# Kernel optimization log

Hardware: AMD Instinct MI355X
Metric: run time of the kernel (lower is better)

Reference implementation:

```python
import jax, jax.numpy as jnp
import numpy as np

DIM, HEADS, HEAD_DIM = 1024, 16, 64
B, S = 2, 1024
LAMBDA = 4.0
EPS = 1e-6


def setup_inputs() -> dict:
    key = jax.random.key(0)
    ks = jax.random.split(key, 7)
    sc = 1.0 / np.sqrt(DIM)
    return {
        "x": jax.random.normal(ks[0], (B, S, DIM), jnp.float32),
        "qkv_w": jax.random.normal(ks[1], (3 * DIM, DIM), jnp.float32) * sc,
        "qkv_b": jax.random.normal(ks[2], (3 * DIM,), jnp.float32) * 0.01,
        "proj_w": jax.random.normal(ks[3], (DIM, DIM), jnp.float32) * sc,
        "proj_b": jax.random.normal(ks[4], (DIM,), jnp.float32) * 0.01,
        "dwc_w": jax.random.normal(ks[5], (DIM, 1, 3), jnp.float32) * 0.3,
        "dwc_b": jax.random.normal(ks[6], (DIM,), jnp.float32) * 0.01,
    }


def _l1_dist(q, k):
    # q,k: [B,H,S,Dh] -> pairwise L1 distance [B,H,S,S].
    # Accumulate over head_dim with a (rematerialized) scan so we never
    # materialize the [B,H,S,S,Dh] broadcast tensor.
    qT = jnp.moveaxis(q, -1, 0)  # [Dh,B,H,S]
    kT = jnp.moveaxis(k, -1, 0)

    def step(acc, qk):
        qd, kd = qk  # [B,H,S]
        return acc + jnp.abs(qd[..., :, None] - kd[..., None, :]), None

    init = jnp.zeros(q.shape[:-1] + (k.shape[-2],), q.dtype)
    dist, _ = jax.lax.scan(jax.checkpoint(step), init, (qT, kT))
    return dist


def reference(x, qkv_w, qkv_b, proj_w, proj_b, dwc_w, dwc_b):
    Bq, Sq, C = x.shape
    # qkv projection -> q,k,v each [B,H,S,Dh]
    qkv = (x @ qkv_w.T + qkv_b).reshape(Bq, Sq, 3, HEADS, HEAD_DIM)
    qkv = jnp.transpose(qkv, (2, 0, 3, 1, 4))
    q, k, v = qkv[0], qkv[1], qkv[2]

    # exact Laplacian (L1-distance) kernel attention, row-normalized
    dist = _l1_dist(q, k)                       # [B,H,S,S]
    kern = jnp.exp(-LAMBDA * dist / HEAD_DIM)   # mean-L1 scaling
    attn = kern / (jnp.sum(kern, axis=-1, keepdims=True) + EPS)
    global_attn = jnp.einsum("bhij,bhjd->bhid", attn, v)

    # depthwise conv1d local branch on v (channel order = head-major)
    v1d = jnp.transpose(v, (0, 1, 3, 2)).reshape(Bq, C, Sq)  # [B,C,S]
    local = jax.lax.conv_general_dilated(
        v1d, dwc_w, window_strides=(1,), padding=((1, 1),),
        feature_group_count=C, dimension_numbers=("NCH", "OIH", "NCH"))
    local = local + dwc_b[None, :, None]
    local = jnp.transpose(local.reshape(Bq, HEADS, HEAD_DIM, Sq), (0, 1, 3, 2))

    y = global_attn + local                      # [B,H,S,Dh]
    y = jnp.transpose(y, (0, 2, 1, 3)).reshape(Bq, Sq, C)
    return y @ proj_w.T + proj_b
```

## Files before the change

kernel.cpp:

```cpp
#include <hip/hip_runtime.h>

#define DIMC 1024
#define HEADS 16
#define HD 64
#define BATCH 2
#define SEQ 1024
#define NQKV 3072

typedef _Float16 f16;
typedef _Float16 half8 __attribute__((ext_vector_type(8)));
typedef _Float16 half4v __attribute__((ext_vector_type(4)));
typedef float floatx4 __attribute__((ext_vector_type(4)));

__device__ __forceinline__ void gld16(const void* g, void* l) {
  __builtin_amdgcn_global_load_lds((const __attribute__((address_space(1))) void*)g,
                                   (__attribute__((address_space(3))) void*)l, 16, 0, 0);
}

__device__ __forceinline__ unsigned sadU8(unsigned a, unsigned b, unsigned c) {
#if __has_builtin(__builtin_amdgcn_sad_u8)
  return __builtin_amdgcn_sad_u8(a, b, c);
#else
  unsigned d;
  asm("v_sad_u8 %0, %1, %2, %3" : "=v"(d) : "v"(a), "v"(b), "v"(c));
  return d;
#endif
}

__global__ __launch_bounds__(256) void cvt_kernel(
    const float* __restrict__ x, const float* __restrict__ wq, const float* __restrict__ wp,
    f16* __restrict__ x16, f16* __restrict__ wq16, f16* __restrict__ wp16)
{
  int bid = blockIdx.x;
  const float* src; f16* dst; int base;
  if (bid < 512)        { src = x;  dst = x16;  base = bid; }
  else if (bid < 1280)  { src = wq; dst = wq16; base = bid - 512; }
  else                  { src = wp; dst = wp16; base = bid - 1280; }
  long long i0 = (long long)base*1024 + threadIdx.x;
#pragma unroll
  for (int k2 = 0; k2 < 4; ++k2) {
    long long i = i0 + k2*256;
    float4 v = ((const float4*)src)[i];
    half4v h; h[0]=(f16)v.x; h[1]=(f16)v.y; h[2]=(f16)v.z; h[3]=(f16)v.w;
    *(half4v*)(dst + i*4) = h;
  }
}

template<int TM, int TN, int BK, int MW, int MODE>
__global__ __launch_bounds__(256, MW) void gemm_kernel(
    const f16* __restrict__ A, const f16* __restrict__ Bw, const float* __restrict__ bias,
    unsigned char* __restrict__ q8, unsigned char* __restrict__ k8, f16* __restrict__ vT,
    float* __restrict__ outp, int K)
{
  constexpr int MT = TM / 32;
  constexpr int NT = TN / 32;
  constexpr int G  = BK / 8;
  __shared__ f16 As[TM*BK];
  __shared__ f16 Bs[TN*BK];
  const int tid = threadIdx.x;
  const int wave = tid >> 6, lane = tid & 63;
  const int lq = lane >> 4, li = lane & 15;
  const int m0 = blockIdx.y * TM, n0 = blockIdx.x * TN;
  const int wm = (wave & 1) * (TM/2), wn = (wave >> 1) * (TN/2);
  floatx4 acc[MT][NT] = {};

  const int kIters = K / BK;
  for (int kt = 0; kt < kIters; ++kt) {
    __syncthreads();
#pragma unroll
    for (int r = 0; r < TM*BK/2048; ++r) {
      int slot = r*256 + tid;
      int row = slot / G, c = slot % G, g = c ^ (row & (G-1));
      gld16(A + (size_t)(m0+row)*K + kt*BK + g*8, As + slot*8);
    }
#pragma unroll
    for (int r = 0; r < TN*BK/2048; ++r) {
      int slot = r*256 + tid;
      int row = slot / G, c = slot % G, g = c ^ (row & (G-1));
      gld16(Bw + (size_t)(n0+row)*K + kt*BK + g*8, Bs + slot*8);
    }
    __syncthreads();
#pragma unroll
    for (int ks = 0; ks < BK/32; ++ks) {
      half8 af[MT], bf[NT];
      int kc = ks*4 + lq;
#pragma unroll
      for (int t = 0; t < MT; ++t) {
        int am = wm + t*16 + li;
        af[t] = *(const half8*)&As[am*BK + (kc ^ (am & (G-1)))*8];
      }
#pragma unroll
      for (int t = 0; t < NT; ++t) {
        int bn = wn + t*16 + li;
        bf[t] = *(const half8*)&Bs[bn*BK + (kc ^ (bn & (G-1)))*8];
      }
#pragma unroll
      for (int mt = 0; mt < MT; ++mt)
#pragma unroll
        for (int nt = 0; nt < NT; ++nt)
          acc[mt][nt] = __builtin_amdgcn_mfma_f32_16x16x32_f16(af[mt], bf[nt], acc[mt][nt], 0, 0, 0);
    }
  }

#pragma unroll
  for (int mt = 0; mt < MT; ++mt) {
#pragma unroll
    for (int nt = 0; nt < NT; ++nt) {
      int f = n0 + wn + nt*16 + li;
      float bb = bias[f];
      if (MODE == 0) {
        int which = f >> 10, cc = f & 1023, h = cc >> 6, d = cc & 63;
        int t0 = m0 + wm + mt*16 + lq*4;
        int b = t0 >> 10, s0 = t0 & 1023;
        if (which == 2) {
          half4v hv;
#pragma unroll
          for (int r = 0; r < 4; ++r) hv[r] = (f16)(acc[mt][nt][r] + bb);
          *(half4v*)&vT[((size_t)((b*HEADS + h)*HD + d))*SEQ + s0] = hv;
        } else {
          unsigned char* dst = (which == 0) ? q8 : k8;
#pragma unroll
          for (int r = 0; r < 4; ++r) {
            float v = acc[mt][nt][r] + bb;
            int u = (int)floorf(v * 16.0f + 128.5f);
            u = u < 0 ? 0 : (u > 255 ? 255 : u);
            dst[((size_t)((b*HEADS + h)*SEQ + s0 + r))*HD + d] = (unsigned char)u;
          }
        }
      } else {
#pragma unroll
        for (int r = 0; r < 4; ++r) {
          int t = m0 + wm + mt*16 + lq*4 + r;
          outp[(size_t)t*DIMC + f] = acc[mt][nt][r] + bb;
        }
      }
    }
  }
}

__global__ __launch_bounds__(256, 4) void attn_kernel(
    const unsigned char* __restrict__ q8g, const unsigned char* __restrict__ k8g,
    const f16* __restrict__ vTg, const float* __restrict__ dwcw, const float* __restrict__ dwcb,
    f16* __restrict__ y16)
{
  __shared__ unsigned char q8s[32*64];
  __shared__ unsigned char k8s[128*64];
  __shared__ f16 vTs[64*128];
  __shared__ f16 sfrag[8*64*8];
  __shared__ float rspart[32*16];
  __shared__ float rowsum[32];

  const int tid = threadIdx.x;
  const int lin = blockIdx.x + 16 * blockIdx.y;
  const int bh = (lin & 7) * 4 + ((lin >> 3) & 3);
  const int i0 = (lin >> 5) * 32;
  const int lane = tid & 63, wave = tid >> 6;
  const int lq = lane >> 4, li = lane & 15;
  const int iL = tid & 15, jt = tid >> 4;
  const int ksj = jt >> 2, qj = jt & 3;

  {
    if (tid < 128)
      gld16(q8g + ((size_t)(bh*SEQ) + i0)*HD + tid*16, q8s + tid*16);
  }
  __syncthreads();

  unsigned qr[2][16];
#pragma unroll
  for (int n = 0; n < 2; ++n)
#pragma unroll
    for (int c4 = 0; c4 < 4; ++c4) {
      uint4 t = *(const uint4*)&q8s[(iL + n*16)*64 + c4*16];
      qr[n][c4*4+0] = t.x; qr[n][c4*4+1] = t.y; qr[n][c4*4+2] = t.z; qr[n][c4*4+3] = t.w;
    }

  float rs[2] = {0.f, 0.f};
  floatx4 pacc[2] = {};

  for (int jb = 0; jb < 8; ++jb) {
    const int j0 = jb * 128;
    __syncthreads();
#pragma unroll
    for (int r = 0; r < 2; ++r) {
      int slot = r*256 + tid;
      gld16(k8g + ((size_t)(bh*SEQ) + j0)*HD + slot*16, k8s + slot*16);
    }
#pragma unroll
    for (int r = 0; r < 4; ++r) {
      int slot = r*256 + tid;
      int d = slot >> 4, c = slot & 15, sc = c ^ (d & 7);
      gld16(vTg + ((size_t)(bh*HD) + d)*SEQ + j0 + sc*8, vTs + slot*8);
    }
    __syncthreads();

    unsigned sacc[2][8] = {};
#pragma unroll
    for (int c4 = 0; c4 < 4; ++c4) {
      uint4 kk[8];
#pragma unroll
      for (int jj = 0; jj < 8; ++jj)
        kk[jj] = *(const uint4*)&k8s[(jt*8 + jj)*64 + c4*16];
#pragma unroll
      for (int n = 0; n < 2; ++n)
#pragma unroll
        for (int jj = 0; jj < 8; ++jj) {
          sacc[n][jj] = sadU8(qr[n][c4*4+0], kk[jj].x, sacc[n][jj]);
          sacc[n][jj] = sadU8(qr[n][c4*4+1], kk[jj].y, sacc[n][jj]);
          sacc[n][jj] = sadU8(qr[n][c4*4+2], kk[jj].z, sacc[n][jj]);
          sacc[n][jj] = sadU8(qr[n][c4*4+3], kk[jj].w, sacc[n][jj]);
        }
    }
#pragma unroll
    for (int n = 0; n < 2; ++n) {
      half8 sv;
#pragma unroll
      for (int jj = 0; jj < 8; ++jj) {
        float sf = exp2f(-0.0056355275f * (float)sacc[n][jj]);
        rs[n] += sf;
        sv[jj] = (f16)sf;
      }
      *(half8*)&sfrag[((n*4 + ksj)*64 + qj*16 + iL)*8] = sv;
    }
    __syncthreads();

#pragma unroll
    for (int ks = 0; ks < 4; ++ks) {
      half8 a0 = *(const half8*)&sfrag[((0*4 + ks)*64 + lane)*8];
      half8 a1 = *(const half8*)&sfrag[((1*4 + ks)*64 + lane)*8];
      int d = wave*16 + li;
      int kc = ks*4 + lq;
      half8 bfr = *(const half8*)&vTs[d*128 + (kc ^ (d & 7))*8];
      pacc[0] = __builtin_amdgcn_mfma_f32_16x16x32_f16(a0, bfr, pacc[0], 0, 0, 0);
      pacc[1] = __builtin_amdgcn_mfma_f32_16x16x32_f16(a1, bfr, pacc[1], 0, 0, 0);
    }
  }

#pragma unroll
  for (int n = 0; n < 2; ++n) rspart[(iL + n*16)*16 + jt] = rs[n];
  __syncthreads();
  if (tid < 32) {
    float s = 0.f;
#pragma unroll
    for (int t = 0; t < 16; ++t) s += rspart[tid*16 + t];
    rowsum[tid] = s + 1e-6f;
  }
  __syncthreads();

  const int b = bh >> 4, h = bh & 15;
  {
    int d = wave*16 + li;
    int c = h*64 + d;
    float w0 = dwcw[c*3+0], w1 = dwcw[c*3+1], w2 = dwcw[c*3+2], cb = dwcb[c];
    const f16* vrow = vTg + ((size_t)(bh*HD) + d)*SEQ;
#pragma unroll
    for (int mt = 0; mt < 2; ++mt) {
      int s0 = i0 + mt*16 + lq*4;
      float vv[6];
#pragma unroll
      for (int e = 0; e < 6; ++e) {
        int s = s0 - 1 + e;
        vv[e] = (s >= 0 && s < SEQ) ? (float)vrow[s] : 0.f;
      }
#pragma unroll
      for (int r = 0; r < 4; ++r) {
        int ii = mt*16 + lq*4 + r;
        float val = pacc[mt][r] / rowsum[ii];
        val += w0*vv[r] + w1*vv[r+1] + w2*vv[r+2] + cb;
        int s = i0 + ii;
        y16[((size_t)(b*SEQ + s))*DIMC + c] = (f16)val;
      }
    }
  }
}

extern "C" void kernel_launch(void* const* d_in, const int* in_sizes, int n_in,
                              void* d_out, int out_size, void* d_ws, size_t ws_size,
                              hipStream_t stream) {
  const float* x      = (const float*)d_in[0];
  const float* qkv_w  = (const float*)d_in[1];
  const float* qkv_b  = (const float*)d_in[2];
  const float* proj_w = (const float*)d_in[3];
  const float* proj_b = (const float*)d_in[4];
  const float* dwc_w  = (const float*)d_in[5];
  const float* dwc_b  = (const float*)d_in[6];
  float* out = (float*)d_out;

  char* ws = (char*)d_ws;
  f16* x16  = (f16*)(ws);
  f16* wq16 = (f16*)(ws + (4ll<<20));
  f16* wp16 = (f16*)(ws + (10ll<<20));
  unsigned char* q8 = (unsigned char*)(ws + (12ll<<20));
  unsigned char* k8 = (unsigned char*)(ws + (14ll<<20));
  f16* vT   = (f16*)(ws + (16ll<<20));
  f16* y16  = (f16*)(ws + (20ll<<20));

  cvt_kernel<<<1536, 256, 0, stream>>>(x, qkv_w, proj_w, x16, wq16, wp16);
  gemm_kernel<128,128,128,2,0><<<dim3(24, 16), 256, 0, stream>>>(x16, wq16, qkv_b, q8, k8, vT, nullptr, DIMC);
  attn_kernel<<<dim3(16, 64), 256, 0, stream>>>(q8, k8, vT, dwc_w, dwc_b, y16);
  gemm_kernel<64,64,128,4,1><<<dim3(16, 32), 256, 0, stream>>>(y16, wp16, proj_b, nullptr, nullptr, nullptr, out, DIMC);
}
```

Baseline: 150.1 us.

## Double-buffer K tiles, load V fragments directly to registers, swizzle K LDS

The attention kernel now double-buffers the K tile in LDS, prefetching the next block while the current one is processed. This drops one of the two barriers per iteration. V is no longer staged through LDS: each lane loads its MFMA B-fragment straight from global memory into registers, and the sfrag buffer is double-buffered so the single remaining barrier is enough. K rows are XOR-swizzled across 16-byte chunks to reduce LDS bank conflicts. The risks are global-load latency on V sitting directly in front of the MFMAs, and the correctness of a single barrier per iteration with async LDS loads.

```diff
diff --git a/kernel.cpp b/kernel.cpp
--- a/kernel.cpp
+++ b/kernel.cpp
@@ -144,9 +144,8 @@
     f16* __restrict__ y16)
 {
   __shared__ unsigned char q8s[32*64];
-  __shared__ unsigned char k8s[128*64];
-  __shared__ f16 vTs[64*128];
-  __shared__ f16 sfrag[8*64*8];
+  __shared__ unsigned char k8s[2][128*64];
+  __shared__ f16 sfrag[2][8*64*8];
   __shared__ float rspart[32*16];
   __shared__ float rowsum[32];
 
@@ -158,10 +157,17 @@
   const int lq = lane >> 4, li = lane & 15;
   const int iL = tid & 15, jt = tid >> 4;
   const int ksj = jt >> 2, qj = jt & 3;
+  const int scs = jt & 3;
 
   {
     if (tid < 128)
       gld16(q8g + ((size_t)(bh*SEQ) + i0)*HD + tid*16, q8s + tid*16);
+#pragma unroll
+    for (int r = 0; r < 2; ++r) {
+      int slot = r*256 + tid;
+      int row = slot >> 2, c4 = slot & 3, sc4 = c4 ^ ((row >> 3) & 3);
+      gld16(k8g + ((size_t)(bh*SEQ) + row)*HD + sc4*16, k8s[0] + slot*16);
+    }
   }
   __syncthreads();
 
@@ -176,22 +182,25 @@
 
   float rs[2] = {0.f, 0.f};
   floatx4 pacc[2] = {};
+  const f16* vbase = vTg + ((size_t)(bh*HD) + wave*16 + li)*SEQ;
 
   for (int jb = 0; jb < 8; ++jb) {
     const int j0 = jb * 128;
-    __syncthreads();
-#pragma unroll
-    for (int r = 0; r < 2; ++r) {
-      int slot = r*256 + tid;
-      gld16(k8g + ((size_t)(bh*SEQ) + j0)*HD + slot*16, k8s + slot*16);
-    }
-#pragma unroll
-    for (int r = 0; r < 4; ++r) {
-      int slot = r*256 + tid;
-      int d = slot >> 4, c = slot & 15, sc = c ^ (d & 7);
-      gld16(vTg + ((size_t)(bh*HD) + d)*SEQ + j0 + sc*8, vTs + slot*8);
-    }
-    __syncthreads();
+    const int cur = jb & 1;
+
+    if (jb < 7) {
+#pragma unroll
+      for (int r = 0; r < 2; ++r) {
+        int slot = r*256 + tid;
+        int row = slot >> 2, c4 = slot & 3, sc4 = c4 ^ ((row >> 3) & 3);
+        gld16(k8g + ((size_t)(bh*SEQ) + j0 + 128 + row)*HD + sc4*16,
+              k8s[cur ^ 1] + slot*16);
+      }
+    }
+    half8 vfrag[4];
+#pragma unroll
+    for (int ks = 0; ks < 4; ++ks)
+      vfrag[ks] = *(const half8*)(vbase + j0 + (ks*4 + lq)*8);
 
     unsigned sacc[2][8] = {};
 #pragma unroll
@@ -199,7 +208,7 @@
       uint4 kk[8];
 #pragma unroll
       for (int jj = 0; jj < 8; ++jj)
-        kk[jj] = *(const uint4*)&k8s[(jt*8 + jj)*64 + c4*16];
+        kk[jj] = *(const uint4*)&k8s[cur][(jt*8 + jj)*64 + ((c4 ^ scs) << 4)];
 #pragma unroll
       for (int n = 0; n < 2; ++n)
 #pragma unroll
@@ -219,19 +228,16 @@
         rs[n] += sf;
         sv[jj] = (f16)sf;
       }
-      *(half8*)&sfrag[((n*4 + ksj)*64 + qj*16 + iL)*8] = sv;
+      *(half8*)&sfrag[cur][((n*4 + ksj)*64 + qj*16 + iL)*8] = sv;
     }
     __syncthreads();
 
 #pragma unroll
     for (int ks = 0; ks < 4; ++ks) {
-      half8 a0 = *(const half8*)&sfrag[((0*4 + ks)*64 + lane)*8];
-      half8 a1 = *(const half8*)&sfrag[((1*4 + ks)*64 + lane)*8];
-      int d = wave*16 + li;
-      int kc = ks*4 + lq;
-      half8 bfr = *(const half8*)&vTs[d*128 + (kc ^ (d & 7))*8];
-      pacc[0] = __builtin_amdgcn_mfma_f32_16x16x32_f16(a0, bfr, pacc[0], 0, 0, 0);
-      pacc[1] = __builtin_amdgcn_mfma_f32_16x16x32_f16(a1, bfr, pacc[1], 0, 0, 0);
+      half8 a0 = *(const half8*)&sfrag[cur][((0*4 + ks)*64 + lane)*8];
+      half8 a1 = *(const half8*)&sfrag[cur][((1*4 + ks)*64 + lane)*8];
+      pacc[0] = __builtin_amdgcn_mfma_f32_16x16x32_f16(a0, vfrag[ks], pacc[0], 0, 0, 0);
+      pacc[1] = __builtin_amdgcn_mfma_f32_16x16x32_f16(a1, vfrag[ks], pacc[1], 0, 0, 0);
     }
   }
 
```

Result: faster. 146.5 us (-2.4%).
